# Performance work log

Measured on AMD Instinct MI355X. Metric: run time of the kernel, lower is better.

## Reference

```python
import jax, jax.numpy as jnp
import numpy as np

B, Q, DIM, HEADS, RPE_H, HGRID, WGRID, STRIDE = 2, 900, 256, 8, 512, 64, 64, 16
KV = HGRID * WGRID


def setup_inputs() -> dict:
    key = jax.random.key(0)
    ks = jax.random.split(key, 16)
    s = 0.02
    return {
        "hidden_states": jax.random.normal(ks[0], (B, Q, DIM), jnp.float32),
        "reference_points": jax.random.uniform(ks[1], (B, Q, 1, 4), jnp.float32),
        "key_value_states": jax.random.normal(ks[2], (B, KV, DIM), jnp.float32),
        "spatial_shapes": jnp.array([[HGRID, WGRID]], dtype=jnp.int64),
        "attention_mask": jax.random.randint(ks[3], (B, KV), 0, 2, jnp.int32),
        "mlp1_w1": jax.random.normal(ks[4], (RPE_H, 2), jnp.float32) * s,
        "mlp1_b1": jnp.zeros((RPE_H,), jnp.float32),
        "mlp1_w2": jax.random.normal(ks[5], (HEADS, RPE_H), jnp.float32) * s,
        "mlp2_w1": jax.random.normal(ks[6], (RPE_H, 2), jnp.float32) * s,
        "mlp2_b1": jnp.zeros((RPE_H,), jnp.float32),
        "mlp2_w2": jax.random.normal(ks[7], (HEADS, RPE_H), jnp.float32) * s,
        "q_w": jax.random.normal(ks[8], (DIM, DIM), jnp.float32) * s,
        "q_b": jnp.zeros((DIM,), jnp.float32),
        "k_w": jax.random.normal(ks[9], (DIM, DIM), jnp.float32) * s,
        "k_b": jnp.zeros((DIM,), jnp.float32),
        "v_w": jax.random.normal(ks[10], (DIM, DIM), jnp.float32) * s,
        "v_b": jnp.zeros((DIM,), jnp.float32),
        "o_w": jax.random.normal(ks[11], (DIM, DIM), jnp.float32) * s,
        "o_b": jnp.zeros((DIM,), jnp.float32),
    }


def _attn(hidden_states, reference_points, key_value_states, h, w, attention_mask,
          mlp1_w1, mlp1_b1, mlp1_w2, mlp2_w1, mlp2_b1, mlp2_w2,
          q_w, q_b, k_w, k_b, v_w, v_b, o_w, o_b):
    b, q_len, dim = hidden_states.shape
    nh = mlp1_w2.shape[0]
    hd = dim // nh
    scale = hd ** -0.5
    stride = STRIDE

    # boxes cxcywh -> x1y1x2y2, scaled to absolute pixel coords (reparam=False)
    c, sz = reference_points[..., :2], reference_points[..., 2:]
    ref = jnp.concatenate([c - sz / 2, c + sz / 2], axis=-1)  # (B,Q,1,4)
    mult = jnp.array([w * stride, h * stride, w * stride, h * stride], dtype=ref.dtype)
    ref = ref * mult

    pos_x = (jnp.arange(w, dtype=jnp.float32) + 0.5) * stride
    pos_y = (jnp.arange(h, dtype=jnp.float32) + 0.5) * stride
    dx = ref[..., 0::2] - pos_x[None, None, :, None]  # (B,Q,W,2)
    dy = ref[..., 1::2] - pos_y[None, None, :, None]  # (B,Q,H,2)

    # small MLPs: 2 -> rpe_hidden -> num_heads
    rpe_x = jax.nn.relu(dx @ mlp1_w1.T + mlp1_b1) @ mlp1_w2.T  # (B,Q,W,nh)
    rpe_y = jax.nn.relu(dy @ mlp2_w1.T + mlp2_b1) @ mlp2_w2.T  # (B,Q,H,nh)
    rpe = rpe_x[:, :, None, :, :] + rpe_y[:, :, :, None, :]    # (B,Q,H,W,nh)
    rpe = rpe.reshape(b, q_len, h * w, nh).transpose(0, 3, 1, 2)  # (B,nh,Q,K)

    queries = (hidden_states @ q_w.T + q_b).reshape(b, q_len, nh, hd).transpose(0, 2, 1, 3) * scale
    kv_len = key_value_states.shape[1]
    keys = (key_value_states @ k_w.T + k_b).reshape(b, kv_len, nh, hd).transpose(0, 2, 1, 3)
    values = (key_value_states @ v_w.T + v_b).reshape(b, kv_len, nh, hd).transpose(0, 2, 1, 3)

    scores = jnp.einsum('bhqd,bhkd->bhqk', queries, keys) + rpe
    scores = scores + attention_mask.astype(scores.dtype)[:, None, None] * (-100.0)
    probs = jax.nn.softmax(scores, axis=-1)
    ctx = jnp.einsum('bhqk,bhkd->bhqd', probs, values)
    ctx = ctx.transpose(0, 2, 1, 3).reshape(b, q_len, dim)
    return ctx @ o_w.T + o_b


def reference(hidden_states, reference_points, key_value_states, spatial_shapes, attention_mask,
              mlp1_w1, mlp1_b1, mlp1_w2, mlp2_w1, mlp2_b1, mlp2_w2,
              q_w, q_b, k_w, k_b, v_w, v_b, o_w, o_b):
    h = int(spatial_shapes[0, 0])
    w = int(spatial_shapes[0, 1])
    return _attn(hidden_states, reference_points, key_value_states, h, w, attention_mask,
                 mlp1_w1, mlp1_b1, mlp1_w2, mlp2_w1, mlp2_b1, mlp2_w2,
                 q_w, q_b, k_w, k_b, v_w, v_b, o_w, o_b)
```

## Files before the change

kernel.cpp:

```cpp
#include <hip/hip_runtime.h>
#include <math.h>

#define NB    2
#define NQ    900
#define NQP   960
#define NKV   4096
#define DIMM  256
#define NHEAD 8
#define HD    32
#define RPEH  512
#define GRID  64
#define SPLIT 4

#define LOG2E 1.4426950408889634f

typedef short short8 __attribute__((ext_vector_type(8)));
typedef float f32x4 __attribute__((ext_vector_type(4)));
typedef unsigned uint2v __attribute__((ext_vector_type(2)));
typedef unsigned short u16;
typedef unsigned short u16x4 __attribute__((ext_vector_type(4)));

__device__ inline u16 f2bf(float f) {
    unsigned u = __builtin_bit_cast(unsigned, f);
    u += 0x7fff + ((u >> 16) & 1);
    return (u16)(u >> 16);
}
__device__ inline unsigned cvtpk_bf16(float a, float b) {
    unsigned r;
    asm("v_cvt_pk_bf16_f32 %0, %1, %2" : "=v"(r) : "v"(a), "v"(b));
    return r;
}

#define HS4  115200
#define KV4  524288
#define W4   16384
#define CONVB 1024
__global__ __launch_bounds__(256) void prep_kernel(
    const float* __restrict__ hs, const float* __restrict__ kv,
    const float* __restrict__ qw, const float* __restrict__ kw,
    const float* __restrict__ vw,
    const float* __restrict__ ref_pts,
    const float* __restrict__ w1x, const float* __restrict__ b1x,
    const float* __restrict__ w2x,
    const float* __restrict__ w1y, const float* __restrict__ b1y,
    const float* __restrict__ w2y,
    u16* __restrict__ hsbf, u16* __restrict__ kvbf,
    u16* __restrict__ qwbf, u16* __restrict__ kwbf, u16* __restrict__ vwbf,
    float* __restrict__ rpex, float* __restrict__ rpey)
{
    __shared__ f32x4 wpk[RPEH];
    __shared__ float w2t[RPEH][NHEAD];
    __shared__ float2 red[3][4][4][64];

    const int t = threadIdx.x;

    if (blockIdx.x < CONVB) {
        const int total = HS4 + KV4 + 3 * W4;
        for (int g = blockIdx.x * 256 + t; g < total; g += CONVB * 256) {
            const float* s; u16* d; int off;
            if (g < HS4)                       { s = hs; d = hsbf; off = g; }
            else if (g < HS4 + KV4)            { s = kv; d = kvbf; off = g - HS4; }
            else if (g < HS4 + KV4 + W4)       { s = qw; d = qwbf; off = g - HS4 - KV4; }
            else if (g < HS4 + KV4 + 2 * W4)   { s = kw; d = kwbf; off = g - HS4 - KV4 - W4; }
            else                               { s = vw; d = vwbf; off = g - HS4 - KV4 - 2 * W4; }
            f32x4 v = *(const f32x4*)(s + (size_t)off * 4);
            *(u16x4*)(d + (size_t)off * 4) =
                (u16x4){f2bf(v[0]), f2bf(v[1]), f2bf(v[2]), f2bf(v[3])};
        }
        return;
    }

    const int bid = blockIdx.x - CONVB;
    const int m   = bid & 1;
    const int bq0 = (bid >> 1) * 4;

    const float* w1 = m ? w1y : w1x;
    const float* b1 = m ? b1y : b1x;
    const float* w2 = m ? w2y : w2x;
    for (int r = t; r < RPEH; r += 256) {
        float a = w1[r * 2], b = w1[r * 2 + 1];
        wpk[r] = (f32x4){a, b, b1[r], a + b};
    }
    for (int i = t; i < RPEH * NHEAD; i += 256) {
        int h = i >> 9, r = i & 511;
        w2t[r][h] = w2[h * RPEH + r] * LOG2E;
    }
    __syncthreads();

    const int lane = t & 63;
    const int wv   = t >> 6;
    const float p  = (lane + 0.5f) * 16.f;

    float lo[4], hi[4];
    #pragma unroll
    for (int j = 0; j < 4; ++j) {
        const float* q = ref_pts + (size_t)(bq0 + j) * 4;
        float c = m ? q[1] : q[0];
        float s = m ? q[3] : q[2];
        lo[j] = (c - s * 0.5f) * 1024.f;
        hi[j] = (c + s * 0.5f) * 1024.f;
    }

    float2 acc[4][4] = {};
    const int r0 = wv * 128;
    #pragma unroll 4
    for (int rr = 0; rr < 128; ++rr) {
        int r = r0 + rr;
        f32x4 W  = wpk[r];
        f32x4 u0 = *(const f32x4*)&w2t[r][0];
        f32x4 u1 = *(const f32x4*)&w2t[r][4];
        float bp = W[3] * p;
        #pragma unroll
        for (int tk = 0; tk < 4; ++tk) {
            float al  = W[0] * lo[tk] + W[1] * hi[tk] + W[2];
            float hid = fmaxf(al - bp, 0.f);
            acc[tk][0].x += u0[0] * hid;  acc[tk][0].y += u0[1] * hid;
            acc[tk][1].x += u0[2] * hid;  acc[tk][1].y += u0[3] * hid;
            acc[tk][2].x += u1[0] * hid;  acc[tk][2].y += u1[1] * hid;
            acc[tk][3].x += u1[2] * hid;  acc[tk][3].y += u1[3] * hid;
        }
    }

    if (wv > 0) {
        #pragma unroll
        for (int tk = 0; tk < 4; ++tk)
            #pragma unroll
            for (int j = 0; j < 4; ++j)
                red[wv - 1][tk][j][lane] = acc[tk][j];
    }
    __syncthreads();
    if (wv == 0) {
        float* outp = m ? rpey : rpex;
        #pragma unroll
        for (int tk = 0; tk < 4; ++tk) {
            size_t base = (size_t)(bq0 + tk) * (NHEAD * GRID) + lane;
            #pragma unroll
            for (int j = 0; j < 4; ++j) {
                float2 s0 = red[0][tk][j][lane];
                float2 s1 = red[1][tk][j][lane];
                float2 s2 = red[2][tk][j][lane];
                float sx = acc[tk][j].x + s0.x + s1.x + s2.x;
                float sy = acc[tk][j].y + s0.y + s1.y + s2.y;
                outp[base + (2 * j) * GRID]     = sx;
                outp[base + (2 * j + 1) * GRID] = sy;
            }
        }
    }
}

__global__ __launch_bounds__(256) void proj_mfma(
    const u16* __restrict__ hsbf, const u16* __restrict__ kvbf,
    const u16* __restrict__ qwbf, const float* __restrict__ q_b,
    const u16* __restrict__ kwbf, const float* __restrict__ k_b,
    const u16* __restrict__ vwbf, const float* __restrict__ v_b,
    u16* __restrict__ Qbf, u16* __restrict__ Kbf, u16* __restrict__ Vt,
    float scaleQ)
{
    __shared__ u16 Abuf[2][4096];
    __shared__ u16 Bbuf[2][4096];

    const u16* A; const u16* W; const float* bias;
    u16* outRow = nullptr; bool vt = false; int M; float scale = 1.f;
    if (blockIdx.z == 0)      { A = kvbf; W = kwbf; bias = k_b; outRow = Kbf; M = NB * NKV; }
    else if (blockIdx.z == 1) { A = kvbf; W = vwbf; bias = v_b; vt = true;   M = NB * NKV; }
    else {
        if (blockIdx.x >= 15) return;
        A = hsbf; W = qwbf; bias = q_b; outRow = Qbf; M = NB * NQ; scale = scaleQ;
    }

    const int t    = threadIdx.x;
    const int lane = t & 63;
    const int w    = t >> 6;
    const int wm   = w >> 1, wn = w & 1;
    const int m0   = blockIdx.x * 128;
    const int n0   = blockIdx.y * 128;

    const int r0 = t >> 2, c0 = t & 3;
    const int r1 = r0 + 64;
    const int s0 = r0 * 4 + (c0 ^ (r0 & 3));
    const int s1 = r1 * 4 + (c0 ^ (r1 & 3));
    const u16* Arow0 = A + (size_t)(m0 + r0) * DIMM + c0 * 8;
    const u16* Arow1 = A + (size_t)(m0 + r1) * DIMM + c0 * 8;
    const u16* Wrow0 = W + (size_t)(n0 + r0) * DIMM + c0 * 8;
    const u16* Wrow1 = W + (size_t)(n0 + r1) * DIMM + c0 * 8;

    const int fr = lane & 15, fkc = lane >> 4;
    int aslot[4], bslot[4];
    #pragma unroll
    for (int f = 0; f < 4; ++f) {
        int ar = wm * 64 + f * 16 + fr;
        int br = wn * 64 + f * 16 + fr;
        aslot[f] = ar * 4 + (fkc ^ (ar & 3));
        bslot[f] = br * 4 + (fkc ^ (br & 3));
    }
    float bv[4];
    #pragma unroll
    for (int f = 0; f < 4; ++f) bv[f] = bias[n0 + wn * 64 + f * 16 + fr];

    f32x4 acc[4][4] = {};

    {
        short8 a0 = *(const short8*)(Arow0);
        short8 a1 = *(const short8*)(Arow1);
        short8 b0 = *(const short8*)(Wrow0);
        short8 b1 = *(const short8*)(Wrow1);
        *(short8*)&Abuf[0][s0 * 8] = a0;
        *(short8*)&Abuf[0][s1 * 8] = a1;
        *(short8*)&Bbuf[0][s0 * 8] = b0;
        *(short8*)&Bbuf[0][s1 * 8] = b1;
    }
    __syncthreads();

    int cur = 0;
    for (int kt = 0; kt < 8; ++kt) {
        short8 na0, na1, nb0, nb1;
        if (kt < 7) {
            int ko = (kt + 1) * 32;
            na0 = *(const short8*)(Arow0 + ko);
            na1 = *(const short8*)(Arow1 + ko);
            nb0 = *(const short8*)(Wrow0 + ko);
            nb1 = *(const short8*)(Wrow1 + ko);
        }
        short8 af[4], bf[4];
        #pragma unroll
        for (int f = 0; f < 4; ++f) {
            af[f] = *(const short8*)&Abuf[cur][aslot[f] * 8];
            bf[f] = *(const short8*)&Bbuf[cur][bslot[f] * 8];
        }
        #pragma unroll
        for (int i = 0; i < 4; ++i)
            #pragma unroll
            for (int j = 0; j < 4; ++j)
                acc[i][j] = __builtin_amdgcn_mfma_f32_16x16x32_bf16(af[i], bf[j], acc[i][j], 0, 0, 0);
        if (kt < 7) {
            *(short8*)&Abuf[cur ^ 1][s0 * 8] = na0;
            *(short8*)&Abuf[cur ^ 1][s1 * 8] = na1;
            *(short8*)&Bbuf[cur ^ 1][s0 * 8] = nb0;
            *(short8*)&Bbuf[cur ^ 1][s1 * 8] = nb1;
        }
        __syncthreads();
        cur ^= 1;
    }

    #pragma unroll
    for (int i = 0; i < 4; ++i) {
        int mbase = m0 + wm * 64 + i * 16 + 4 * fkc;
        #pragma unroll
        for (int j = 0; j < 4; ++j) {
            int n = n0 + wn * 64 + j * 16 + fr;
            #pragma unroll
            for (int r = 0; r < 4; ++r) {
                int gm = mbase + r;
                if (gm < M) {
                    float v = (acc[i][j][r] + bv[j]) * scale;
                    if (!vt) {
                        outRow[(size_t)gm * DIMM + n] = f2bf(v);
                    } else {
                        int bb = gm >> 12, kvi = gm & 4095;
                        int hh = n >> 5, dd = n & 31;
                        Vt[(size_t)((bb * NHEAD + hh) * HD + dd) * NKV + kvi] = f2bf(v);
                    }
                }
            }
        }
    }
}

__global__ __launch_bounds__(256) void attn_mfma(
    const u16* __restrict__ Qbf, const u16* __restrict__ Kbf,
    const u16* __restrict__ Vt,
    const float* __restrict__ RX, const float* __restrict__ RY,
    const int* __restrict__ mask,
    float* __restrict__ pctx, float2* __restrict__ pml)
{
    constexpr int KSEG = NKV / SPLIT;
    constexpr int NTS  = KSEG / 64;
    __shared__ short8 kbuf[2][4][64];
    __shared__ short8 vbuf[2][4][64];
    __shared__ unsigned pbuf[4][64][4];
    __shared__ float ry_s[NTS][68];
    __shared__ float mbuf[2][64];

    const int tid  = threadIdx.x;
    const int lane = tid & 63;
    const int w    = tid >> 6;
    const int q15  = lane & 15;
    const int g    = lane >> 4;
    const int qt = blockIdx.x, h = blockIdx.y;
    const int b  = blockIdx.z / SPLIT;
    const int sp = blockIdx.z % SPLIT;
    const int q0 = qt * 64;
    const int wq = w * 16 + q15;
    const int gq = q0 + wq;
    const bool qok = gq < NQ;
    const int kv0g = sp * KSEG;

    float rxr[16];
    {
        const float* rxrow = RX + (size_t)(b * NQ + (qok ? gq : 0)) * (NHEAD * GRID) + h * GRID;
        #pragma unroll
        for (int kt = 0; kt < 4; ++kt)
            #pragma unroll
            for (int r = 0; r < 4; ++r)
                rxr[kt * 4 + r] = qok ? rxrow[16 * kt + 4 * g + r] : 0.f;
    }
    for (int idx = tid; idx < NTS * 64; idx += 256) {
        int y = idx & (NTS - 1), q = idx / NTS;
        int gq2 = q0 + q;
        ry_s[y][q] = (gq2 < NQ)
            ? RY[(size_t)(b * NQ + gq2) * (NHEAD * GRID) + h * GRID + sp * NTS + y] : 0.f;
    }

    short8 qf = *(const short8*)(Qbf + ((size_t)(b * NQ + gq)) * DIMM + h * HD + 8 * g);

    const int sr = tid >> 2, sc = tid & 3;
    const int vd = tid >> 3, vc = tid & 7;
    const size_t kbase = ((size_t)(b * NKV + kv0g + sr)) * DIMM + h * HD + 8 * sc;
    const size_t vbase = ((size_t)((b * NHEAD + h) * HD + vd)) * NKV + kv0g + 8 * vc;

    kbuf[0][sr >> 4][(sr & 15) + 16 * sc] = *(const short8*)(Kbf + kbase);
    vbuf[0][(vc >> 2) * 2 + (vd >> 4)][16 * (vc & 3) + (vd & 15)] = *(const short8*)(Vt + vbase);
    if (tid < 64) mbuf[0][tid] = -(100.f * LOG2E) * (float)mask[b * NKV + kv0g + tid];
    __syncthreads();

    f32x4 cacc0 = {0.f, 0.f, 0.f, 0.f};
    f32x4 cacc1 = {0.f, 0.f, 0.f, 0.f};
    float m_run = -1e30f, l_run = 0.f;
    int cur = 0;

    for (int t = 0; t < NTS; ++t) {
        short8 rk = {}, rv = {};
        float rm = 0.f;
        if (t < NTS - 1) {
            size_t kvn = (size_t)(t + 1) * 64;
            rk = *(const short8*)(Kbf + kbase + kvn * DIMM);
            rv = *(const short8*)(Vt + vbase + kvn);
            if (tid < 64) rm = -(100.f * LOG2E) * (float)mask[b * NKV + kv0g + kvn + tid];
        }

        f32x4 zero = {0.f, 0.f, 0.f, 0.f};
        f32x4 s[4];
        __builtin_amdgcn_s_setprio(1);
        #pragma unroll
        for (int kt = 0; kt < 4; ++kt)
            s[kt] = __builtin_amdgcn_mfma_f32_16x16x32_bf16(kbuf[cur][kt][lane], qf, zero, 0, 0, 0);
        __builtin_amdgcn_s_setprio(0);

        float ryb = ry_s[t][wq];
        #pragma unroll
        for (int kt = 0; kt < 4; ++kt) {
            #pragma unroll
            for (int r = 0; r < 4; ++r)
                s[kt][r] += rxr[kt * 4 + r] + ryb + mbuf[cur][16 * kt + 4 * g + r];
        }

        float mk[4];
        #pragma unroll
        for (int kt = 0; kt < 4; ++kt)
            mk[kt] = fmaxf(fmaxf(s[kt][0], s[kt][1]), fmaxf(s[kt][2], s[kt][3]));
        float mloc = fmaxf(fmaxf(mk[0], mk[1]), fmaxf(mk[2], mk[3]));
        mloc = fmaxf(mloc, __shfl_xor(mloc, 16));
        mloc = fmaxf(mloc, __shfl_xor(mloc, 32));

        if (!__all(mloc <= m_run + 8.f)) {
            float mnew = fmaxf(m_run, mloc);
            float fsc  = exp2f(m_run - mnew);
            l_run *= fsc;
            cacc0 *= fsc;
            cacc1 *= fsc;
            m_run = mnew;
        }

        float psum = 0.f;
        #pragma unroll
        for (int kt = 0; kt < 4; ++kt)
            #pragma unroll
            for (int r = 0; r < 4; ++r) {
                float pv = exp2f(s[kt][r] - m_run);
                s[kt][r] = pv;
                psum += pv;
            }
        psum += __shfl_xor(psum, 16);
        psum += __shfl_xor(psum, 32);
        l_run += psum;

        __builtin_amdgcn_s_setprio(1);
        #pragma unroll
        for (int sk = 0; sk < 2; ++sk) {
            #pragma unroll
            for (int kk = 0; kk < 2; ++kk) {
                int kt = sk * 2 + kk;
                unsigned d0 = cvtpk_bf16(s[kt][0], s[kt][1]);
                unsigned d1 = cvtpk_bf16(s[kt][2], s[kt][3]);
                int lt = 16 * ((2 * kt + (g >> 1)) & 3) + q15;
                uint2v* dst = (uint2v*)&pbuf[w][lt][2 * (g & 1)];
                *dst = (uint2v){d0, d1};
            }
            short8 pf = *(const short8*)&pbuf[w][lane][0];
            cacc0 = __builtin_amdgcn_mfma_f32_16x16x32_bf16(vbuf[cur][sk * 2 + 0][lane], pf, cacc0, 0, 0, 0);
            cacc1 = __builtin_amdgcn_mfma_f32_16x16x32_bf16(vbuf[cur][sk * 2 + 1][lane], pf, cacc1, 0, 0, 0);
        }
        __builtin_amdgcn_s_setprio(0);

        if (t < NTS - 1) {
            kbuf[cur ^ 1][sr >> 4][(sr & 15) + 16 * sc] = rk;
            vbuf[cur ^ 1][(vc >> 2) * 2 + (vd >> 4)][16 * (vc & 3) + (vd & 15)] = rv;
            if (tid < 64) mbuf[cur ^ 1][tid] = rm;
        }
        __syncthreads();
        cur ^= 1;
    }

    size_t prow = (size_t)(sp * NB + b) * NQP + gq;
    float* pc = pctx + prow * DIMM + h * HD;
    #pragma unroll
    for (int r = 0; r < 4; ++r) {
        pc[4 * g + r]      = cacc0[r];
        pc[16 + 4 * g + r] = cacc1[r];
    }
    if (g == 0) {
        float2 v; v.x = m_run; v.y = l_run;
        pml[prow * NHEAD + h] = v;
    }
}

__global__ __launch_bounds__(256) void attn_reduce(
    const float* __restrict__ pctx, const float2* __restrict__ pml,
    float* __restrict__ CTX)
{
    const int bq = blockIdx.x;
    const int b = bq / NQ, q = bq - b * NQ;
    const int c = threadIdx.x;
    const int h = c >> 5;

    float m[SPLIT], l[SPLIT];
    #pragma unroll
    for (int sp = 0; sp < SPLIT; ++sp) {
        float2 v = pml[((size_t)(sp * NB + b) * NQP + q) * NHEAD + h];
        m[sp] = v.x; l[sp] = v.y;
    }
    float ms = fmaxf(fmaxf(m[0], m[1]), fmaxf(m[2], m[3]));
    float L = 0.f, acc = 0.f;
    #pragma unroll
    for (int sp = 0; sp < SPLIT; ++sp) {
        float wgt = exp2f(m[sp] - ms);
        L   += wgt * l[sp];
        acc += wgt * pctx[((size_t)(sp * NB + b) * NQP + q) * DIMM + c];
    }
    CTX[(size_t)bq * DIMM + c] = acc / L;
}

__global__ __launch_bounds__(256) void gemm_bias_f32(
    const float* __restrict__ A, const float* __restrict__ W,
    const float* __restrict__ bias, float* __restrict__ C,
    int M, int N, int K)
{
    __shared__ float As[32][33];
    __shared__ float Ws[32][33];
    const int t  = threadIdx.x;
    const int tr = t >> 4;
    const int tc = t & 15;
    const int brow = blockIdx.y * 32;
    const int bcol = blockIdx.x * 32;
    float acc00 = 0.f, acc01 = 0.f, acc10 = 0.f, acc11 = 0.f;

    for (int kt = 0; kt < K; kt += 32) {
        #pragma unroll
        for (int i = 0; i < 4; ++i) {
            int idx = t + i * 256;
            int r = idx >> 5, c = idx & 31;
            int gr = brow + r;
            As[r][c] = (gr < M) ? A[(size_t)gr * K + kt + c] : 0.f;
            Ws[r][c] = W[(size_t)(bcol + r) * K + kt + c];
        }
        __syncthreads();
        #pragma unroll 8
        for (int k = 0; k < 32; ++k) {
            float a0 = As[tr * 2][k], a1 = As[tr * 2 + 1][k];
            float w0 = Ws[tc * 2][k], w1 = Ws[tc * 2 + 1][k];
            acc00 += a0 * w0; acc01 += a0 * w1;
            acc10 += a1 * w0; acc11 += a1 * w1;
        }
        __syncthreads();
    }
    int gc0 = bcol + tc * 2, gc1 = gc0 + 1;
    int gr0 = brow + tr * 2, gr1 = gr0 + 1;
    if (gr0 < M) {
        C[(size_t)gr0 * N + gc0] = acc00 + bias[gc0];
        C[(size_t)gr0 * N + gc1] = acc01 + bias[gc1];
    }
    if (gr1 < M) {
        C[(size_t)gr1 * N + gc0] = acc10 + bias[gc0];
        C[(size_t)gr1 * N + gc1] = acc11 + bias[gc1];
    }
}

extern "C" void kernel_launch(void* const* d_in, const int* in_sizes, int n_in,
                              void* d_out, int out_size, void* d_ws, size_t ws_size,
                              hipStream_t stream)
{
    const float* hs   = (const float*)d_in[0];
    const float* rp   = (const float*)d_in[1];
    const float* kv   = (const float*)d_in[2];
    const int*   msk  = (const int*)d_in[4];
    const float* m1w1 = (const float*)d_in[5];
    const float* m1b1 = (const float*)d_in[6];
    const float* m1w2 = (const float*)d_in[7];
    const float* m2w1 = (const float*)d_in[8];
    const float* m2b1 = (const float*)d_in[9];
    const float* m2w2 = (const float*)d_in[10];
    const float* q_w  = (const float*)d_in[11];
    const float* q_b  = (const float*)d_in[12];
    const float* k_w  = (const float*)d_in[13];
    const float* k_b  = (const float*)d_in[14];
    const float* v_w  = (const float*)d_in[15];
    const float* v_b  = (const float*)d_in[16];
    const float* o_w  = (const float*)d_in[17];
    const float* o_b  = (const float*)d_in[18];
    float* out = (float*)d_out;

    char* p = (char*)d_ws;
    float* RX   = (float*)p; p += (size_t)NB * NQ * NHEAD * GRID * 4;
    float* RY   = (float*)p; p += (size_t)NB * NQ * NHEAD * GRID * 4;
    float* CTX  = (float*)p; p += (size_t)NB * NQ * DIMM * 4;
    u16*   Qbf  = (u16*)p;   p += (size_t)1920 * DIMM * 2;
    u16*   Kbf  = (u16*)p;   p += (size_t)NB * NKV * DIMM * 2;
    u16*   Vt   = (u16*)p;   p += (size_t)NB * NHEAD * HD * NKV * 2;

    char* u = p;
    u16* hsbf = (u16*)u;
    u16* kvbf = hsbf + (size_t)1920 * DIMM;
    u16* qwbf = kvbf + (size_t)NB * NKV * DIMM;
    u16* kwbf = qwbf + (size_t)DIMM * DIMM;
    u16* vwbf = kwbf + (size_t)DIMM * DIMM;
    float*  pctx = (float*)u;
    float2* pml  = (float2*)(pctx + (size_t)SPLIT * NB * NQP * DIMM);

    const float scale = 0.17677669529663687f * LOG2E;

    prep_kernel<<<CONVB + 900, 256, 0, stream>>>(
        hs, kv, q_w, k_w, v_w, rp, m1w1, m1b1, m1w2, m2w1, m2b1, m2w2,
        hsbf, kvbf, qwbf, kwbf, vwbf, RX, RY);

    proj_mfma<<<dim3(64, 2, 3), 256, 0, stream>>>(
        hsbf, kvbf, qwbf, q_b, kwbf, k_b, vwbf, v_b, Qbf, Kbf, Vt, scale);

    attn_mfma<<<dim3((NQ + 63) / 64, NHEAD, NB * SPLIT), 256, 0, stream>>>(
        Qbf, Kbf, Vt, RX, RY, msk, pctx, pml);

    attn_reduce<<<NB * NQ, 256, 0, stream>>>(pctx, pml, CTX);

    gemm_bias_f32<<<dim3(DIMM / 32, (NB * NQ + 31) / 32), 256, 0, stream>>>(
        CTX, o_w, o_b, out, NB * NQ, DIMM, DIMM);
}
```

Baseline: 129.3 us.

## Process 128 keys per attention iteration and read RY directly from global

```diff
diff --git a/kernel.cpp b/kernel.cpp
--- a/kernel.cpp
+++ b/kernel.cpp
@@ -274,12 +274,11 @@
     float* __restrict__ pctx, float2* __restrict__ pml)
 {
     constexpr int KSEG = NKV / SPLIT;
-    constexpr int NTS  = KSEG / 64;
-    __shared__ short8 kbuf[2][4][64];
-    __shared__ short8 vbuf[2][4][64];
+    constexpr int NIT  = KSEG / 128;
+    __shared__ short8 kbuf[2][8][64];
+    __shared__ short8 vbuf[2][8][64];
     __shared__ unsigned pbuf[4][64][4];
-    __shared__ float ry_s[NTS][68];
-    __shared__ float mbuf[2][64];
+    __shared__ float mbuf[2][128];
 
     const int tid  = threadIdx.x;
     const int lane = tid & 63;
@@ -304,12 +303,7 @@
             for (int r = 0; r < 4; ++r)
                 rxr[kt * 4 + r] = qok ? rxrow[16 * kt + 4 * g + r] : 0.f;
     }
-    for (int idx = tid; idx < NTS * 64; idx += 256) {
-        int y = idx & (NTS - 1), q = idx / NTS;
-        int gq2 = q0 + q;
-        ry_s[y][q] = (gq2 < NQ)
-            ? RY[(size_t)(b * NQ + gq2) * (NHEAD * GRID) + h * GRID + sp * NTS + y] : 0.f;
-    }
+    const float* yrow = RY + (size_t)(b * NQ + (qok ? gq : 0)) * (NHEAD * GRID) + h * GRID + sp * 16;
 
     short8 qf = *(const short8*)(Qbf + ((size_t)(b * NQ + gq)) * DIMM + h * HD + 8 * g);
 
@@ -318,9 +312,15 @@
     const size_t kbase = ((size_t)(b * NKV + kv0g + sr)) * DIMM + h * HD + 8 * sc;
     const size_t vbase = ((size_t)((b * NHEAD + h) * HD + vd)) * NKV + kv0g + 8 * vc;
 
-    kbuf[0][sr >> 4][(sr & 15) + 16 * sc] = *(const short8*)(Kbf + kbase);
-    vbuf[0][(vc >> 2) * 2 + (vd >> 4)][16 * (vc & 3) + (vd & 15)] = *(const short8*)(Vt + vbase);
-    if (tid < 64) mbuf[0][tid] = -(100.f * LOG2E) * (float)mask[b * NKV + kv0g + tid];
+    {
+        kbuf[0][sr >> 4][(sr & 15) + 16 * sc] = *(const short8*)(Kbf + kbase);
+        int sr2 = sr + 64;
+        kbuf[0][sr2 >> 4][(sr2 & 15) + 16 * sc] = *(const short8*)(Kbf + kbase + (size_t)64 * DIMM);
+        vbuf[0][(vc >> 2) * 2 + (vd >> 4)][16 * (vc & 3) + (vd & 15)] = *(const short8*)(Vt + vbase);
+        int vc2 = vc + 8;
+        vbuf[0][(vc2 >> 2) * 2 + (vd >> 4)][16 * (vc2 & 3) + (vd & 15)] = *(const short8*)(Vt + vbase + 64);
+        if (tid < 128) mbuf[0][tid] = -(100.f * LOG2E) * (float)mask[b * NKV + kv0g + tid];
+    }
     __syncthreads();
 
     f32x4 cacc0 = {0.f, 0.f, 0.f, 0.f};
@@ -328,37 +328,42 @@
     float m_run = -1e30f, l_run = 0.f;
     int cur = 0;
 
-    for (int t = 0; t < NTS; ++t) {
-        short8 rk = {}, rv = {};
+    for (int t = 0; t < NIT; ++t) {
+        short8 rk0 = {}, rk1 = {}, rv0 = {}, rv1 = {};
         float rm = 0.f;
-        if (t < NTS - 1) {
-            size_t kvn = (size_t)(t + 1) * 64;
-            rk = *(const short8*)(Kbf + kbase + kvn * DIMM);
-            rv = *(const short8*)(Vt + vbase + kvn);
-            if (tid < 64) rm = -(100.f * LOG2E) * (float)mask[b * NKV + kv0g + kvn + tid];
-        }
+        if (t < NIT - 1) {
+            size_t kvn = (size_t)(t + 1) * 128;
+            rk0 = *(const short8*)(Kbf + kbase + kvn * DIMM);
+            rk1 = *(const short8*)(Kbf + kbase + (kvn + 64) * DIMM);
+            rv0 = *(const short8*)(Vt + vbase + kvn);
+            rv1 = *(const short8*)(Vt + vbase + kvn + 64);
+            if (tid < 128) rm = -(100.f * LOG2E) * (float)mask[b * NKV + kv0g + kvn + tid];
+        }
+        float ryb0 = qok ? yrow[2 * t] : 0.f;
+        float ryb1 = qok ? yrow[2 * t + 1] : 0.f;
 
         f32x4 zero = {0.f, 0.f, 0.f, 0.f};
-        f32x4 s[4];
+        f32x4 s[8];
         __builtin_amdgcn_s_setprio(1);
         #pragma unroll
-        for (int kt = 0; kt < 4; ++kt)
+        for (int kt = 0; kt < 8; ++kt)
             s[kt] = __builtin_amdgcn_mfma_f32_16x16x32_bf16(kbuf[cur][kt][lane], qf, zero, 0, 0, 0);
         __builtin_amdgcn_s_setprio(0);
 
-        float ryb = ry_s[t][wq];
-        #pragma unroll
-        for (int kt = 0; kt < 4; ++kt) {
+        #pragma unroll
+        for (int kt = 0; kt < 8; ++kt) {
+            float ryb = (kt < 4) ? ryb0 : ryb1;
             #pragma unroll
             for (int r = 0; r < 4; ++r)
-                s[kt][r] += rxr[kt * 4 + r] + ryb + mbuf[cur][16 * kt + 4 * g + r];
-        }
-
-        float mk[4];
-        #pragma unroll
-        for (int kt = 0; kt < 4; ++kt)
+                s[kt][r] += rxr[(kt & 3) * 4 + r] + ryb + mbuf[cur][16 * kt + 4 * g + r];
+        }
+
+        float mk[8];
+        #pragma unroll
+        for (int kt = 0; kt < 8; ++kt)
             mk[kt] = fmaxf(fmaxf(s[kt][0], s[kt][1]), fmaxf(s[kt][2], s[kt][3]));
-        float mloc = fmaxf(fmaxf(mk[0], mk[1]), fmaxf(mk[2], mk[3]));
+        float mloc = fmaxf(fmaxf(fmaxf(mk[0], mk[1]), fmaxf(mk[2], mk[3])),
+                           fmaxf(fmaxf(mk[4], mk[5]), fmaxf(mk[6], mk[7])));
         mloc = fmaxf(mloc, __shfl_xor(mloc, 16));
         mloc = fmaxf(mloc, __shfl_xor(mloc, 32));
 
@@ -373,7 +378,7 @@
 
         float psum = 0.f;
         #pragma unroll
-        for (int kt = 0; kt < 4; ++kt)
+        for (int kt = 0; kt < 8; ++kt)
             #pragma unroll
             for (int r = 0; r < 4; ++r) {
                 float pv = exp2f(s[kt][r] - m_run);
@@ -386,7 +391,7 @@
 
         __builtin_amdgcn_s_setprio(1);
         #pragma unroll
-        for (int sk = 0; sk < 2; ++sk) {
+        for (int sk = 0; sk < 4; ++sk) {
             #pragma unroll
             for (int kk = 0; kk < 2; ++kk) {
                 int kt = sk * 2 + kk;
@@ -402,10 +407,14 @@
         }
         __builtin_amdgcn_s_setprio(0);
 
-        if (t < NTS - 1) {
-            kbuf[cur ^ 1][sr >> 4][(sr & 15) + 16 * sc] = rk;
-            vbuf[cur ^ 1][(vc >> 2) * 2 + (vd >> 4)][16 * (vc & 3) + (vd & 15)] = rv;
-            if (tid < 64) mbuf[cur ^ 1][tid] = rm;
+        if (t < NIT - 1) {
+            kbuf[cur ^ 1][sr >> 4][(sr & 15) + 16 * sc] = rk0;
+            int sr2 = sr + 64;
+            kbuf[cur ^ 1][sr2 >> 4][(sr2 & 15) + 16 * sc] = rk1;
+            vbuf[cur ^ 1][(vc >> 2) * 2 + (vd >> 4)][16 * (vc & 3) + (vd & 15)] = rv0;
+            int vc2 = vc + 8;
+            vbuf[cur ^ 1][(vc2 >> 2) * 2 + (vd >> 4)][16 * (vc2 & 3) + (vd & 15)] = rv1;
+            if (tid < 128) mbuf[cur ^ 1][tid] = rm;
         }
         __syncthreads();
         cur ^= 1;
```

Measured after the change: 137.8 us. +6.6%, slower.
